# Optimization experiments

Hardware: AMD Instinct MI355X
Metric: run time of the kernel (lower is better)

The kernel has to match this reference:

```python
import jax, jax.numpy as jnp
import numpy as np

B, IN_UNITS, IN_CHANNELS, NUM_UNITS, UNIT_SIZE = 128, 32, 4096, 10, 16
NUM_ITER = 3


def setup_inputs() -> dict:
    key = jax.random.key(0)
    k1, k2 = jax.random.split(key)
    # x: primary-capsule output [B, in_units, in_channels]
    x = jax.random.normal(k1, (B, IN_UNITS, IN_CHANNELS), dtype=jnp.float32)
    # W: routing weights, torch param shape [1, C, J, D, K] with batch dim dropped
    W = jax.random.normal(k2, (IN_CHANNELS, NUM_UNITS, UNIT_SIZE, IN_UNITS), dtype=jnp.float32)
    return {"x": x, "W": W}


def reference(x, W):
    b_sz = x.shape[0]
    C, J = W.shape[0], W.shape[1]
    # torch: x.transpose(1,2) -> [B,C,K]; u_hat = W @ x -> [B,C,J,D,1]
    # u_hat[b,i,j,d] = sum_k W[i,j,d,k] * x[b,k,i]
    u_hat = jnp.einsum('ijdk,bki->bijd', W, x)  # [B, C, J, D]
    b_ij = jnp.zeros((C, J), dtype=x.dtype)
    v = None
    for _ in range(NUM_ITER):
        # faithful: softmax over dim=1 (in_channels axis), not over classes
        c_ij = jax.nn.softmax(b_ij, axis=0)               # [C, J]
        s = jnp.einsum('ij,bijd->bjd', c_ij, u_hat)        # [B, J, D]
        # faithful squash: original sums over dim=2 of [B,1,J,D,1] == class axis J
        mag_sq = jnp.sum(s * s, axis=1, keepdims=True)     # [B, 1, D]
        v = (mag_sq / (1.0 + mag_sq)) * (s / jnp.sqrt(mag_sq))
        # agreement: <u_hat, v> averaged over batch
        agree = jnp.einsum('bijd,bjd->ij', u_hat, v) / b_sz
        b_ij = b_ij + agree
    # torch returns v_j.squeeze(1): [B, J, D, 1]
    return v[:, :, :, None]
```

## Files before the change

### kernel.cpp

```cpp
#include <hip/hip_runtime.h>


typedef __attribute__((ext_vector_type(8))) __bf16 bf16x8;
typedef __attribute__((ext_vector_type(4))) float  f32x4;
typedef __attribute__((ext_vector_type(8))) unsigned short u16x8;
typedef __attribute__((ext_vector_type(4))) unsigned short u16x4;

#define DI __device__ __forceinline__

DI float bf2f(unsigned short u){ unsigned int x = ((unsigned int)u) << 16; return __builtin_bit_cast(float, x); }
DI unsigned short f2bf(float f){
  unsigned int u = __builtin_bit_cast(unsigned int, f);
  u += 0x7fffu + ((u >> 16) & 1u);
  return (unsigned short)(u >> 16);
}

constexpr int Ci = 4096, Kk = 32, Jj = 10, Dd = 16, Bb = 128;
constexpr int KI = Ci * Kk;
constexpr int JDt = Jj * Dd;
constexpr int NCH = 256, CK = 512;

constexpr size_t OFF_XB = 0;
constexpr size_t SZ_XB  = (size_t)Bb * KI * 2;
constexpr size_t OFF_W2 = OFF_XB + SZ_XB;
constexpr size_t SZ_W2  = (size_t)JDt * KI * 2;
constexpr size_t OFF_BT = OFF_W2 + SZ_W2;
constexpr size_t SZ_BT  = (size_t)Jj * Ci * 4;
constexpr size_t OFF_CT = OFF_BT + SZ_BT;
constexpr size_t OFF_VBT = OFF_CT + SZ_BT;
constexpr size_t SZ_VBT = (size_t)JDt * Bb * 2;
constexpr size_t OFF_SP = OFF_VBT + SZ_VBT;
constexpr size_t SZ_SP  = (size_t)NCH * Bb * JDt * 4;

__global__ __launch_bounds__(256) void pack_all(const float* __restrict__ x, const float* __restrict__ W,
                                                unsigned short* __restrict__ xbf, unsigned short* __restrict__ w2,
                                                float* __restrict__ bT){
  __shared__ float tile[64][65];
  const int bid = blockIdx.x;
  if(bid < 5120){
    const int mt = bid % 80, it = bid / 80;
    const int m0 = mt * 64, i0 = it * 64;
    #pragma unroll
    for(int u=0; u<4; u++){
      int e = threadIdx.x + 256*u;
      int il = e >> 4, q = e & 15;
      float4 v = *(const float4*)(W + (size_t)(i0+il)*5120 + m0 + q*4);
      tile[il][q*4+0]=v.x; tile[il][q*4+1]=v.y; tile[il][q*4+2]=v.z; tile[il][q*4+3]=v.w;
    }
    __syncthreads();
    #pragma unroll
    for(int u=0; u<4; u++){
      int e = threadIdx.x + 256*u;
      int ml = e >> 4, q = e & 15;
      u16x4 o;
      o[0]=f2bf(tile[q*4+0][ml]); o[1]=f2bf(tile[q*4+1][ml]);
      o[2]=f2bf(tile[q*4+2][ml]); o[3]=f2bf(tile[q*4+3][ml]);
      *(u16x4*)(w2 + (size_t)(m0+ml)*Ci + i0 + q*4) = o;
    }
  } else if(bid < 13312){
    const size_t e = (size_t)(bid - 5120) * 256 + threadIdx.x;
    const float4* xv = (const float4*)x;
    float4 a = xv[e*2], b = xv[e*2+1];
    u16x8 o;
    o[0]=f2bf(a.x); o[1]=f2bf(a.y); o[2]=f2bf(a.z); o[3]=f2bf(a.w);
    o[4]=f2bf(b.x); o[5]=f2bf(b.y); o[6]=f2bf(b.z); o[7]=f2bf(b.w);
    *(u16x8*)(xbf + e*8) = o;
  } else {
    const int zb = bid - 13312;
    ((float4*)bT)[zb*256 + threadIdx.x] = float4{0.f,0.f,0.f,0.f};
  }
}

__global__ __launch_bounds__(256) void softmax_k(const float* __restrict__ bT, float* __restrict__ cT){
  const int j = blockIdx.x, tid = threadIdx.x, lane = tid & 63, wid = tid >> 6;
  __shared__ float red[4];
  float vals[16];
  float mx = -3.4e38f;
  #pragma unroll
  for(int u=0; u<16; u++){ vals[u] = bT[j*Ci + tid + 256*u]; mx = fmaxf(mx, vals[u]); }
  #pragma unroll
  for(int o=32; o>0; o>>=1) mx = fmaxf(mx, __shfl_xor(mx, o));
  if(lane == 0) red[wid] = mx;
  __syncthreads();
  mx = fmaxf(fmaxf(red[0],red[1]), fmaxf(red[2],red[3]));
  float sm = 0.f;
  #pragma unroll
  for(int u=0; u<16; u++){ vals[u] = expf(vals[u]-mx); sm += vals[u]; }
  #pragma unroll
  for(int o=32; o>0; o>>=1) sm += __shfl_xor(sm, o);
  __syncthreads();
  if(lane == 0) red[wid] = sm;
  __syncthreads();
  sm = red[0]+red[1]+red[2]+red[3];
  float inv = 1.0f / sm;
  #pragma unroll
  for(int u=0; u<16; u++) cT[j*Ci + tid + 256*u] = vals[u]*inv;
}

__global__ __launch_bounds__(512) void s_pass(const unsigned short* __restrict__ xb,
                                              const unsigned short* __restrict__ w2,
                                              const float* __restrict__ cT,
                                              float* __restrict__ spart){
  __shared__ unsigned short xs[128*64];
  __shared__ unsigned short wsm[160*64];
  const int tid = threadIdx.x, lane = tid & 63, wid = tid >> 6;
  const int wb = wid & 3, wj = wid >> 2;
  const int ki0 = blockIdx.x * CK;
  f32x4 acc[2][5];
  const f32x4 z = {0.f,0.f,0.f,0.f};
  #pragma unroll
  for(int m=0;m<2;m++){ acc[m][0]=z; acc[m][1]=z; acc[m][2]=z; acc[m][3]=z; acc[m][4]=z; }

  for(int step=0; step<CK/64; ++step){
    const int kb = ki0 + step*64;
    const int ib = kb & (Ci-1);
    #pragma unroll
    for(int u=0; u<2; u++){
      int e = tid + 512*u;
      int b = e >> 3, sg = e & 7;
      u16x8 v = *(const u16x8*)(xb + (size_t)b*KI + kb + sg*8);
      *(u16x8*)((char*)xs + b*128 + ((sg*16) ^ ((b&7)<<4))) = v;
    }
    #pragma unroll
    for(int u=0; u<3; u++){
      int e = tid + 512*u;
      if(e < 1280){
        int jd = e >> 3, sg = e & 7;
        u16x8 v = *(const u16x8*)(w2 + (size_t)jd*KI + kb + sg*8);
        float cc[8];
        if(cT){
          const float* cp = cT + (jd>>4)*Ci + ib + sg*8;
          float4 c0 = *(const float4*)cp;
          float4 c1 = *(const float4*)(cp+4);
          cc[0]=c0.x; cc[1]=c0.y; cc[2]=c0.z; cc[3]=c0.w;
          cc[4]=c1.x; cc[5]=c1.y; cc[6]=c1.z; cc[7]=c1.w;
        } else {
          #pragma unroll
          for(int q=0;q<8;q++) cc[q] = (1.0f/4096.0f);
        }
        u16x8 o;
        #pragma unroll
        for(int q=0;q<8;q++) o[q] = f2bf(bf2f(v[q])*cc[q]);
        *(u16x8*)((char*)wsm + jd*128 + ((sg*16) ^ ((jd&7)<<4))) = o;
      }
    }
    __syncthreads();
    #pragma unroll
    for(int ks=0; ks<2; ks++){
      const int kk2 = (ks*32 + ((lane>>4)<<3)) * 2;
      bf16x8 a[2];
      #pragma unroll
      for(int m=0;m<2;m++){
        int row = wb*32 + m*16 + (lane&15);
        a[m] = *(const bf16x8*)((const char*)xs + row*128 + (kk2 ^ ((row&7)<<4)));
      }
      #pragma unroll
      for(int n=0;n<5;n++){
        int row = wj*80 + n*16 + (lane&15);
        bf16x8 bb = *(const bf16x8*)((const char*)wsm + row*128 + (kk2 ^ ((row&7)<<4)));
        acc[0][n] = __builtin_amdgcn_mfma_f32_16x16x32_bf16(a[0], bb, acc[0][n], 0,0,0);
        acc[1][n] = __builtin_amdgcn_mfma_f32_16x16x32_bf16(a[1], bb, acc[1][n], 0,0,0);
      }
    }
    __syncthreads();
  }
  float* sp = spart + (size_t)blockIdx.x * (Bb*JDt);
  #pragma unroll
  for(int m=0;m<2;m++)
    #pragma unroll
    for(int n=0;n<5;n++)
      #pragma unroll
      for(int r=0;r<4;r++){
        int b  = wb*32 + m*16 + ((lane>>4)<<2) + r;
        int jd = wj*80 + n*16 + (lane&15);
        sp[b*JDt + jd] = acc[m][n][r];
      }
}

__global__ __launch_bounds__(256) void redsq(const float* __restrict__ spart,
                                             float* __restrict__ vout,
                                             unsigned short* __restrict__ vbT){
  const int b = blockIdx.x, tid = threadIdx.x;
  __shared__ float sq[JDt];
  __shared__ float scale[Dd];
  float s = 0.f;
  if(tid < JDt){
    const float* p = spart + b*JDt + tid;
    #pragma unroll 8
    for(int ch=0; ch<NCH; ch++) s += p[(size_t)ch*(Bb*JDt)];
    sq[tid] = s*s;
  }
  __syncthreads();
  if(tid < Dd){
    float m = 0.f;
    #pragma unroll
    for(int j=0;j<Jj;j++) m += sq[j*Dd + tid];
    scale[tid] = sqrtf(m) / (1.0f + m);
  }
  __syncthreads();
  if(tid < JDt){
    float v = s * scale[tid & (Dd-1)];
    vout[b*JDt + tid] = v;
    vbT[tid*Bb + b] = f2bf(v);
  }
}

__global__ __launch_bounds__(256) void agree_pass(const unsigned short* __restrict__ xb,
                                                  const unsigned short* __restrict__ vbT,
                                                  const unsigned short* __restrict__ w2,
                                                  float* __restrict__ bT){
  __shared__ unsigned short xsT[64*128];
  __shared__ unsigned short vsm[160*128];
  const int tid = threadIdx.x, lane = tid & 63, wid = tid >> 6;
  const int wj = wid & 1, wk = wid >> 1;
  const int ki0 = blockIdx.x * 64;
  #pragma unroll
  for(int u=0; u<4; u++){
    int e = tid + 256*u;
    int b = e >> 3, sg = e & 7;
    u16x8 v = *(const u16x8*)(xb + (size_t)b*KI + ki0 + sg*8);
    #pragma unroll
    for(int q=0; q<8; q++){
      int kil = sg*8 + q;
      *(unsigned short*)((char*)xsT + kil*256 + ((b*2) ^ ((kil&7)<<4))) = v[q];
    }
  }
  #pragma unroll
  for(int u=0; u<10; u++){
    int e = tid + 256*u;
    int jd = e >> 4, sg = e & 15;
    u16x8 v = *(const u16x8*)(vbT + jd*Bb + sg*8);
    *(u16x8*)((char*)vsm + jd*256 + ((sg*16) ^ ((jd&7)<<4))) = v;
  }
  __syncthreads();
  f32x4 acc[5][2];
  const f32x4 z = {0.f,0.f,0.f,0.f};
  #pragma unroll
  for(int m=0;m<5;m++){ acc[m][0]=z; acc[m][1]=z; }
  #pragma unroll
  for(int ks=0; ks<4; ks++){
    const int b2 = (ks*32 + ((lane>>4)<<3)) * 2;
    bf16x8 bfr[2];
    #pragma unroll
    for(int n=0;n<2;n++){
      int row = wk*32 + n*16 + (lane&15);
      bfr[n] = *(const bf16x8*)((const char*)xsT + row*256 + (b2 ^ ((row&7)<<4)));
    }
    #pragma unroll
    for(int m=0;m<5;m++){
      int row = wj*80 + m*16 + (lane&15);
      bf16x8 af = *(const bf16x8*)((const char*)vsm + row*256 + (b2 ^ ((row&7)<<4)));
      acc[m][0] = __builtin_amdgcn_mfma_f32_16x16x32_bf16(af, bfr[0], acc[m][0], 0,0,0);
      acc[m][1] = __builtin_amdgcn_mfma_f32_16x16x32_bf16(af, bfr[1], acc[m][1], 0,0,0);
    }
  }
  const int ibase = ki0 & (Ci-1);
  #pragma unroll
  for(int m=0;m<5;m++){
    int j = wj*5 + m;
    #pragma unroll
    for(int n=0;n<2;n++){
      int colg = ki0 + wk*32 + n*16 + (lane&15);
      float s = 0.f;
      #pragma unroll
      for(int r=0;r<4;r++){
        int jdrow = wj*80 + m*16 + ((lane>>4)<<2) + r;
        s += acc[m][n][r] * bf2f(w2[(size_t)jdrow*KI + colg]);
      }
      s += __shfl_xor(s, 16);
      s += __shfl_xor(s, 32);
      if(lane < 16){
        int ig = ibase + wk*32 + n*16 + lane;
        atomicAdd(bT + j*Ci + ig, s * (1.0f/128.0f));
      }
    }
  }
}

extern "C" void kernel_launch(void* const* d_in, const int* in_sizes, int n_in,
                              void* d_out, int out_size, void* d_ws, size_t ws_size,
                              hipStream_t stream) {
  const float* x = (const float*)d_in[0];
  const float* W = (const float*)d_in[1];
  float* out = (float*)d_out;
  char* ws = (char*)d_ws;
  unsigned short* xbf = (unsigned short*)(ws + OFF_XB);
  unsigned short* w2  = (unsigned short*)(ws + OFF_W2);
  float* bT           = (float*)(ws + OFF_BT);
  float* cT           = (float*)(ws + OFF_CT);
  unsigned short* vbT = (unsigned short*)(ws + OFF_VBT);
  float* spart        = (float*)(ws + OFF_SP);

  pack_all<<<13352, 256, 0, stream>>>(x, W, xbf, w2, bT);
  for(int t=0; t<3; t++){
    if(t > 0) softmax_k<<<Jj, 256, 0, stream>>>(bT, cT);
    s_pass<<<NCH, 512, 0, stream>>>(xbf, w2, (t==0)? nullptr : cT, spart);
    redsq<<<Bb, 256, 0, stream>>>(spart, out, vbT);
    if(t < 2) agree_pass<<<KI/64, 256, 0, stream>>>(xbf, vbT, w2, bT);
  }
}
```

Before: 228.4 us.

## Split packing kernel, use hardware bf16 pack conversion and wider transpose tiles

The single fused pack kernel is split into a W-transpose kernel and an x-convert/zero kernel. The W transpose now uses 64x512 tiles stored as bf16 in shared memory, and it writes 16-byte rows instead of 8-byte ones. Float-to-bf16 conversion switches from software rounding to the v_cvt_pk_bf16_f32 instruction. The aim is to cut preprocessing cost through wider stores and cheaper conversion, at the price of one extra launch and 16-bit LDS reads with possible bank conflicts.

Measured after the change: 229.7 us. No clear change (+0.6%).

```diff
diff --git a/kernel.cpp b/kernel.cpp
--- a/kernel.cpp
+++ b/kernel.cpp
@@ -4,7 +4,7 @@
 typedef __attribute__((ext_vector_type(8))) __bf16 bf16x8;
 typedef __attribute__((ext_vector_type(4))) float  f32x4;
 typedef __attribute__((ext_vector_type(8))) unsigned short u16x8;
-typedef __attribute__((ext_vector_type(4))) unsigned short u16x4;
+typedef __attribute__((ext_vector_type(4))) unsigned int  u32x4;
 
 #define DI __device__ __forceinline__
 
@@ -13,6 +13,11 @@
   unsigned int u = __builtin_bit_cast(unsigned int, f);
   u += 0x7fffu + ((u >> 16) & 1u);
   return (unsigned short)(u >> 16);
+}
+DI unsigned int cvtpk(float lo, float hi){
+  unsigned int r;
+  asm("v_cvt_pk_bf16_f32 %0, %1, %2" : "=v"(r) : "v"(lo), "v"(hi));
+  return r;
 }
 
 constexpr int Ci = 4096, Kk = 32, Jj = 10, Dd = 16, Bb = 128;
@@ -32,43 +37,50 @@
 constexpr size_t OFF_SP = OFF_VBT + SZ_VBT;
 constexpr size_t SZ_SP  = (size_t)NCH * Bb * JDt * 4;
 
-__global__ __launch_bounds__(256) void pack_all(const float* __restrict__ x, const float* __restrict__ W,
-                                                unsigned short* __restrict__ xbf, unsigned short* __restrict__ w2,
-                                                float* __restrict__ bT){
-  __shared__ float tile[64][65];
+constexpr int WPAD = 522;
+__global__ __launch_bounds__(512) void pack_w(const float* __restrict__ W, unsigned short* __restrict__ w2){
+  __shared__ unsigned short t16[64 * WPAD];
+  const int mt = blockIdx.x % 10, it = blockIdx.x / 10;
+  const int m0 = mt * 512, i0 = it * 64;
+  #pragma unroll
+  for(int u=0; u<16; u++){
+    int e = threadIdx.x + 512*u;
+    int row = e >> 7, c4 = e & 127;
+    float4 v = *(const float4*)(W + (size_t)(i0+row)*5120 + m0 + c4*4);
+    unsigned int* p = (unsigned int*)(t16 + row*WPAD + c4*4);
+    p[0] = cvtpk(v.x, v.y);
+    p[1] = cvtpk(v.z, v.w);
+  }
+  __syncthreads();
+  #pragma unroll
+  for(int u=0; u<8; u++){
+    int e = threadIdx.x + 512*u;
+    int mr = e >> 3, g = e & 7;
+    u32x4 o;
+    #pragma unroll
+    for(int j=0; j<4; j++){
+      unsigned int lo = t16[(g*8 + 2*j    )*WPAD + mr];
+      unsigned int hi = t16[(g*8 + 2*j + 1)*WPAD + mr];
+      o[j] = lo | (hi << 16);
+    }
+    *(u32x4*)(w2 + (size_t)(m0+mr)*Ci + i0 + g*8) = o;
+  }
+}
+
+__global__ __launch_bounds__(256) void pack_x(const float* __restrict__ x, unsigned short* __restrict__ xbf,
+                                              float* __restrict__ bT){
   const int bid = blockIdx.x;
-  if(bid < 5120){
-    const int mt = bid % 80, it = bid / 80;
-    const int m0 = mt * 64, i0 = it * 64;
-    #pragma unroll
-    for(int u=0; u<4; u++){
-      int e = threadIdx.x + 256*u;
-      int il = e >> 4, q = e & 15;
-      float4 v = *(const float4*)(W + (size_t)(i0+il)*5120 + m0 + q*4);
-      tile[il][q*4+0]=v.x; tile[il][q*4+1]=v.y; tile[il][q*4+2]=v.z; tile[il][q*4+3]=v.w;
-    }
-    __syncthreads();
-    #pragma unroll
-    for(int u=0; u<4; u++){
-      int e = threadIdx.x + 256*u;
-      int ml = e >> 4, q = e & 15;
-      u16x4 o;
-      o[0]=f2bf(tile[q*4+0][ml]); o[1]=f2bf(tile[q*4+1][ml]);
-      o[2]=f2bf(tile[q*4+2][ml]); o[3]=f2bf(tile[q*4+3][ml]);
-      *(u16x4*)(w2 + (size_t)(m0+ml)*Ci + i0 + q*4) = o;
-    }
-  } else if(bid < 13312){
-    const size_t e = (size_t)(bid - 5120) * 256 + threadIdx.x;
-    const float4* xv = (const float4*)x;
-    float4 a = xv[e*2], b = xv[e*2+1];
-    u16x8 o;
-    o[0]=f2bf(a.x); o[1]=f2bf(a.y); o[2]=f2bf(a.z); o[3]=f2bf(a.w);
-    o[4]=f2bf(b.x); o[5]=f2bf(b.y); o[6]=f2bf(b.z); o[7]=f2bf(b.w);
-    *(u16x8*)(xbf + e*8) = o;
-  } else {
-    const int zb = bid - 13312;
-    ((float4*)bT)[zb*256 + threadIdx.x] = float4{0.f,0.f,0.f,0.f};
-  }
+  if(bid >= 8192){
+    ((f32x4*)bT)[(bid-8192)*256 + threadIdx.x] = f32x4{0.f,0.f,0.f,0.f};
+    return;
+  }
+  const size_t e = (size_t)bid * 256 + threadIdx.x;
+  const float4* xv = (const float4*)x;
+  float4 a = xv[e*2], b = xv[e*2+1];
+  u32x4 o;
+  o[0]=cvtpk(a.x,a.y); o[1]=cvtpk(a.z,a.w);
+  o[2]=cvtpk(b.x,b.y); o[3]=cvtpk(b.z,b.w);
+  *(u32x4*)(xbf + e*8) = o;
 }
 
 __global__ __launch_bounds__(256) void softmax_k(const float* __restrict__ bT, float* __restrict__ cT){
@@ -291,7 +303,8 @@
   unsigned short* vbT = (unsigned short*)(ws + OFF_VBT);
   float* spart        = (float*)(ws + OFF_SP);
 
-  pack_all<<<13352, 256, 0, stream>>>(x, W, xbf, w2, bT);
+  pack_w<<<640, 512, 0, stream>>>(W, w2);
+  pack_x<<<8232, 256, 0, stream>>>(x, xbf, bT);
   for(int t=0; t<3; t++){
     if(t > 0) softmax_k<<<Jj, 256, 0, stream>>>(bT, cT);
     s_pass<<<NCH, 512, 0, stream>>>(xbf, w2, (t==0)? nullptr : cT, spart);
```
